# Kernel optimization log

Hardware: AMD Instinct MI355X
Metric: run time of the kernel (lower is better)

## Reference

```python
import jax, jax.numpy as jnp
import numpy as np

B, D, N, L, H, T = 256, 768, 256, 2, 8, 20
HD = D // H

def _ln(x, g, b):
    m = x.mean(-1, keepdims=True)
    v = ((x - m) ** 2).mean(-1, keepdims=True)
    return (x - m) / jnp.sqrt(v + 1e-5) * g + b

def setup_inputs() -> dict:
    key = jax.random.key(0)
    ks = jax.random.split(key, 8)
    kk = jax.random.split(ks[7], 10)
    def w(k, shape):
        return jax.random.normal(k, shape, jnp.float32) * 0.02
    return {
        'feats': jax.random.normal(ks[0], (B, D, N), jnp.float32),
        'past': jax.random.normal(ks[1], (B, 16, 6), jnp.float32),
        'w_qinit': w(ks[2], (121, D)), 'b_qinit': jnp.zeros((D,), jnp.float32),
        'pos_enc': w(ks[3], (1, N, D)),
        'w_pp': w(ks[4], (2, D)), 'b_pp': jnp.zeros((D,), jnp.float32),
        'g_pp': jnp.ones((D,), jnp.float32), 'be_pp': jnp.zeros((D,), jnp.float32),
        'time_emb': w(ks[5], (T, D)),
        'Wq': w(kk[0], (L, D, D)), 'bq': jnp.zeros((L, D), jnp.float32),
        'Wk': w(kk[1], (L, D, D)), 'bk': jnp.zeros((L, D), jnp.float32),
        'Wv': w(kk[2], (L, D, D)), 'bv': jnp.zeros((L, D), jnp.float32),
        'Wo': w(kk[3], (L, D, D)), 'bo': jnp.zeros((L, D), jnp.float32),
        'ln1_g': jnp.ones((L, D), jnp.float32), 'ln1_b': jnp.zeros((L, D), jnp.float32),
        'W1': w(kk[4], (L, D, 4 * D)), 'b1': jnp.zeros((L, 4 * D), jnp.float32),
        'W2': w(kk[5], (L, 4 * D, D)), 'b2': jnp.zeros((L, D), jnp.float32),
        'ln2_g': jnp.ones((L, D), jnp.float32), 'ln2_b': jnp.zeros((L, D), jnp.float32),
        'w_dec1': w(kk[6], (D, D)), 'b_dec1': jnp.zeros((D,), jnp.float32),
        'w_dec2': w(kk[7], (D, 2)), 'b_dec2': jnp.zeros((2,), jnp.float32),
        'intent': jax.random.randint(ks[6], (B,), 0, 3),
    }

def reference(feats, past, w_qinit, b_qinit, pos_enc, w_pp, b_pp, g_pp, be_pp,
              time_emb, Wq, bq, Wk, bk, Wv, bv, Wo, bo, ln1_g, ln1_b,
              W1, b1, W2, b2, ln2_g, ln2_b, w_dec1, b_dec1, w_dec2, b_dec2, intent):
    # tokens: [B, N, D]
    tokens = jnp.transpose(feats, (0, 2, 1)) + pos_enc
    onehot = jax.nn.one_hot(jnp.clip(intent - 1, 0, 2), 3, dtype=tokens.dtype)
    past_flat = past.reshape(B, -1)
    pad = jnp.zeros((B, 22), tokens.dtype)
    context = jnp.concatenate([onehot, past_flat, pad], axis=1) @ w_qinit + b_qinit  # [B, D]
    # precompute cross-attention K/V once per layer (tokens are constant across steps)
    Kh = (jnp.einsum('bnd,lde->lbne', tokens, Wk) + bk[:, None, None, :]).reshape(L, B, N, H, HD)
    Vh = (jnp.einsum('bnd,lde->lbne', tokens, Wv) + bv[:, None, None, :]).reshape(L, B, N, H, HD)
    scale = 1.0 / np.sqrt(HD)

    def step(carry, te):
        ctx, cp = carry
        pq = jax.nn.relu(_ln(cp @ w_pp + b_pp, g_pp, be_pp))
        x = (ctx + pq + te)[:, None, :]  # [B, 1, D]
        for l in range(L):
            q = (_ln(x, ln1_g[l], ln1_b[l]) @ Wq[l] + bq[l]).reshape(B, 1, H, HD)
            s = jnp.einsum('bqhd,bnhd->bhqn', q, Kh[l]) * scale
            a = jax.nn.softmax(s, axis=-1)
            o = jnp.einsum('bhqn,bnhd->bqhd', a, Vh[l]).reshape(B, 1, D) @ Wo[l] + bo[l]
            x = x + o
            h = jax.nn.gelu(_ln(x, ln2_g[l], ln2_b[l]) @ W1[l] + b1[l], approximate=False) @ W2[l] + b2[l]
            x = x + h
        ctx = x[:, 0]
        delta = jax.nn.gelu(ctx @ w_dec1 + b_dec1, approximate=False) @ w_dec2 + b_dec2
        cp = cp + delta
        return (ctx, cp), cp

    init = (context, past[:, -1, 0:2])
    _, ys = jax.lax.scan(step, init, time_emb)  # ys: [T, B, 2]
    return jnp.transpose(ys, (1, 0, 2))
```

## Files before the change

kernel.cpp:

```cpp
#include <hip/hip_runtime.h>
#include <hip/hip_bf16.h>
#include <math.h>

#define B_ 256
#define D_ 768
#define N_ 256
#define L_ 2
#define H_ 8
#define T_ 20
#define HD_ 96
#define D4_ 3072

typedef float f32x4v __attribute__((ext_vector_type(4)));
typedef __bf16 bf16x8v __attribute__((ext_vector_type(8)));

union V16 { uint4 u; bf16x8v v; };

__device__ __forceinline__ ushort f2b(float f) {
    union { float f; unsigned u; } x{f};
    unsigned r = x.u + 0x7fffu + ((x.u >> 16) & 1u);
    return (ushort)(r >> 16);
}
__device__ __forceinline__ float b2f(ushort s) {
    union { unsigned u; float f; } x{(unsigned)s << 16};
    return x.f;
}
__device__ __forceinline__ float gelu_f(float v) {
    return 0.5f * v * (1.0f + erff(v * 0.7071067811865476f));
}
__device__ __forceinline__ float dot8(const float* __restrict__ xp, uint4 u) {
    return xp[0] * b2f((ushort)(u.x & 0xffffu)) + xp[1] * b2f((ushort)(u.x >> 16))
         + xp[2] * b2f((ushort)(u.y & 0xffffu)) + xp[3] * b2f((ushort)(u.y >> 16))
         + xp[4] * b2f((ushort)(u.z & 0xffffu)) + xp[5] * b2f((ushort)(u.z >> 16))
         + xp[6] * b2f((ushort)(u.w & 0xffffu)) + xp[7] * b2f((ushort)(u.w >> 16));
}
__device__ __forceinline__ float blockSum(float v, float* red, int tid) {
    for (int off = 32; off; off >>= 1) v += __shfl_down(v, off, 64);
    int w = tid >> 6, lane = tid & 63;
    if (lane == 0) red[w] = v;
    __syncthreads();
    float r = red[0] + red[1] + red[2] + red[3];
    __syncthreads();
    return r;
}
__device__ __forceinline__ void gl_lds16(const ushort* g, ushort* l) {
    __builtin_amdgcn_global_load_lds((const __attribute__((address_space(1))) unsigned int*)g,
                                     (__attribute__((address_space(3))) unsigned int*)l,
                                     16, 0, 0);
}

__global__ __launch_bounds__(256) void context_kernel(const float* __restrict__ past,
                                                      const float* __restrict__ w_qinit,
                                                      const float* __restrict__ b_qinit,
                                                      const int* __restrict__ intent,
                                                      const float* __restrict__ w_pp,
                                                      const float* __restrict__ b_pp,
                                                      const float* __restrict__ g_pp,
                                                      const float* __restrict__ be_pp,
                                                      const float* __restrict__ te0,
                                                      float* __restrict__ x,
                                                      float* __restrict__ cp) {
    int b = blockIdx.x, tid = threadIdx.x;
    __shared__ float ps[96];
    __shared__ int oidx;
    __shared__ float red[4];
    if (tid < 96) ps[tid] = past[b * 96 + tid];
    if (tid == 0) {
        int iv = intent[b] - 1;
        oidx = iv < 0 ? 0 : (iv > 2 ? 2 : iv);
    }
    __syncthreads();
    float ctx[3];
    #pragma unroll
    for (int r = 0; r < 3; ++r) {
        int d = tid + r * 256;
        float acc = w_qinit[oidx * D_ + d] + b_qinit[d];
        #pragma unroll 8
        for (int p = 0; p < 96; ++p) acc += ps[p] * w_qinit[(3 + p) * D_ + d];
        ctx[r] = acc;
    }
    float c0 = ps[90], c1 = ps[91];
    if (tid == 0) { cp[b * 2] = c0; cp[b * 2 + 1] = c1; }
    float t[3];
    float s = 0, ss = 0;
    #pragma unroll
    for (int r = 0; r < 3; ++r) {
        int d = tid + r * 256;
        t[r] = c0 * w_pp[d] + c1 * w_pp[D_ + d] + b_pp[d];
        s += t[r]; ss += t[r] * t[r];
    }
    s = blockSum(s, red, tid);
    ss = blockSum(ss, red, tid);
    float mean = s * (1.0f / D_);
    float var = ss * (1.0f / D_) - mean * mean;
    float rinv = rsqrtf(var + 1e-5f);
    #pragma unroll
    for (int r = 0; r < 3; ++r) {
        int d = tid + r * 256;
        float pq = fmaxf((t[r] - mean) * rinv * g_pp[d] + be_pp[d], 0.0f);
        x[b * D_ + d] = ctx[r] + pq + te0[d];
    }
}

__global__ __launch_bounds__(256) void token_prep(const float* __restrict__ feats,
                                                  const float* __restrict__ pos_enc,
                                                  ushort* __restrict__ tokens) {
    int b = blockIdx.z;
    int d0 = blockIdx.x * 64, n0 = blockIdx.y * 64;
    __shared__ float tile[64][65];
    int tid = threadIdx.x;
    int nl = tid & 63, dl0 = tid >> 6;
    const float* fb = feats + ((size_t)b * D_ + d0) * N_ + n0;
    #pragma unroll
    for (int i = 0; i < 16; ++i) {
        int dl = dl0 + i * 4;
        tile[dl][nl] = fb[(size_t)dl * N_ + nl];
    }
    __syncthreads();
    int dq = (tid & 15) * 4;
    int ng = tid >> 4;
    #pragma unroll
    for (int i = 0; i < 4; ++i) {
        int nl2 = ng + i * 16;
        int n = n0 + nl2;
        float4 p = *(const float4*)(pos_enc + (size_t)n * D_ + d0 + dq);
        ushort4 o;
        o.x = f2b(tile[dq + 0][nl2] + p.x);
        o.y = f2b(tile[dq + 1][nl2] + p.y);
        o.z = f2b(tile[dq + 2][nl2] + p.z);
        o.w = f2b(tile[dq + 3][nl2] + p.w);
        *(ushort4*)&tokens[((size_t)b * N_ + n) * D_ + d0 + dq] = o;
    }
}

__global__ __launch_bounds__(256) void transpose_w(const float* __restrict__ W,
                                                   ushort* __restrict__ out,
                                                   const float* __restrict__ scale,
                                                   int K, int N) {
    __shared__ float t[32][33];
    int k0 = blockIdx.y * 32, n0 = blockIdx.x * 32;
    int tx = threadIdx.x & 31, ty = threadIdx.x >> 5;
    #pragma unroll
    for (int i = 0; i < 4; ++i)
        t[ty + i * 8][tx] = W[(size_t)(k0 + ty + i * 8) * N + n0 + tx];
    __syncthreads();
    #pragma unroll
    for (int i = 0; i < 4; ++i) {
        int n = n0 + ty + i * 8, k = k0 + tx;
        float v = t[tx][ty + i * 8];
        if (scale) v *= scale[k];
        out[(size_t)n * K + k] = f2b(v);
    }
}

__global__ __launch_bounds__(256) void bias_eff_kernel(const float* __restrict__ W,
                                                       const float* __restrict__ bias,
                                                       const float* __restrict__ lb,
                                                       float* __restrict__ be, int Nc) {
    __shared__ float lbs[768];
    __shared__ float part[4][64];
    int tid = threadIdx.x;
    for (int i = tid; i < 768; i += 256) lbs[i] = lb[i];
    __syncthreads();
    int n0 = blockIdx.x * 64;
    int nl = tid & 63, kp = tid >> 6;
    int n = n0 + nl;
    float a = 0.0f;
    #pragma unroll 4
    for (int k = kp * 192; k < kp * 192 + 192; ++k)
        a += lbs[k] * W[(size_t)k * Nc + n];
    part[kp][nl] = a;
    __syncthreads();
    if (tid < 64)
        be[n0 + tid] = bias[n0 + tid] + part[0][tid] + part[1][tid] + part[2][tid] + part[3][tid];
}

__global__ void kvbias_prep(const float* __restrict__ bk, const float* __restrict__ bv,
                            float* __restrict__ bc) {
    int i = blockIdx.x * 256 + threadIdx.x;
    int mi = i / D_, c = i % D_;
    int l = mi >> 1;
    bc[i] = (mi & 1 ? bv : bk)[l * D_ + c];
}

__global__ __launch_bounds__(256) void kv_gemm_mfma(const ushort* __restrict__ tokens,
                                                    const ushort* __restrict__ Wkvt,
                                                    const float* __restrict__ bias_kv,
                                                    ushort* __restrict__ Kt,
                                                    ushort* __restrict__ Vt) {
    int e0 = blockIdx.x * 128;
    int mi = e0 / D_;
    int ein = e0 % D_;
    int l = mi >> 1, isV = mi & 1;
    int m0 = blockIdx.y * 128;
    int b = m0 >> 8, ntok0 = m0 & 255;
    __shared__ __align__(16) ushort smem[17408];
    int tid = threadIdx.x;
    int w = tid >> 6, lane = tid & 63, quad = lane >> 4, l16 = lane & 15;
    int wr = w >> 1, wc = w & 1;
    int swz = (l16 >> 1) & 3;
    int rchunk = ((quad ^ swz) & 3) * 8;
    f32x4v acc[4][4];
    #pragma unroll
    for (int i = 0; i < 4; ++i)
        #pragma unroll
        for (int j = 0; j < 4; ++j) acc[i][j] = (f32x4v)(0.0f);

    auto stage = [&](int buf, int k0) {
        ushort* Ab = smem + buf * 8192;
        ushort* Bb = Ab + 4096;
        #pragma unroll
        for (int vv = 0; vv < 2; ++vv) {
            int v = tid + vv * 256;
            int row = v >> 2;
            int kq = (v & 3) ^ ((row >> 1) & 3);
            gl_lds16(&tokens[(size_t)(m0 + row) * D_ + k0 + kq * 8], Ab + w * 512 + vv * 2048);
            gl_lds16(&Wkvt[(size_t)(e0 + row) * D_ + k0 + kq * 8],   Bb + w * 512 + vv * 2048);
        }
    };

    stage(0, 0);
    asm volatile("s_waitcnt vmcnt(0)" ::: "memory");
    __syncthreads();
    int cur = 0;
    for (int k0 = 0; k0 < D_; k0 += 32) {
        if (k0 + 32 < D_) stage(cur ^ 1, k0 + 32);
        const ushort* Ab = smem + cur * 8192;
        const ushort* Bb = Ab + 4096;
        V16 a[4], bb[4];
        #pragma unroll
        for (int i = 0; i < 4; ++i)
            a[i].u = *(const uint4*)&Ab[(wr * 64 + i * 16 + l16) * 32 + rchunk];
        #pragma unroll
        for (int j = 0; j < 4; ++j)
            bb[j].u = *(const uint4*)&Bb[(wc * 64 + j * 16 + l16) * 32 + rchunk];
        #pragma unroll
        for (int i = 0; i < 4; ++i)
            #pragma unroll
            for (int j = 0; j < 4; ++j)
                acc[i][j] = __builtin_amdgcn_mfma_f32_16x16x32_bf16(a[i].v, bb[j].v, acc[i][j], 0, 0, 0);
        asm volatile("s_waitcnt vmcnt(0)" ::: "memory");
        __syncthreads();
        cur ^= 1;
    }

    float bcol[4];
    #pragma unroll
    for (int j = 0; j < 4; ++j)
        bcol[j] = bias_kv[e0 + wc * 64 + j * 16 + l16];

    ushort* Ct = smem;
    ushort* outbuf = isV ? Vt : Kt;
    #pragma unroll
    for (int i = 0; i < 4; ++i)
        #pragma unroll
        for (int j = 0; j < 4; ++j) {
            int e_l = wc * 64 + j * 16 + l16;
            int m_b = wr * 64 + i * 16 + quad * 4;
            ushort4 p;
            p.x = f2b(acc[i][j][0] + bcol[j]);
            p.y = f2b(acc[i][j][1] + bcol[j]);
            p.z = f2b(acc[i][j][2] + bcol[j]);
            p.w = f2b(acc[i][j][3] + bcol[j]);
            *(ushort4*)&Ct[e_l * 136 + m_b] = p;
        }
    __syncthreads();
    int e_l = tid >> 1, half = tid & 1;
    int c = ein + e_l;
    int h = c / HD_, hd = c % HD_;
    size_t dst = ((((size_t)l * B_ + b) * H_ + h) * HD_ + hd) * N_ + ntok0 + half * 64;
    #pragma unroll
    for (int p8 = 0; p8 < 8; ++p8)
        *(uint4*)&outbuf[dst + p8 * 8] = *(const uint4*)&Ct[e_l * 136 + half * 64 + p8 * 8];
}

template<int AVAR, int OMODE, int STATS, int KSPLIT>
__global__ __launch_bounds__(256) void gemm_s(const void* __restrict__ Av,
                                              const ushort* __restrict__ Bt,
                                              const float* __restrict__ bias,
                                              void* __restrict__ Cv,
                                              int K, int Nc) {
    __shared__ __align__(16) ushort As[2][2048];
    __shared__ __align__(16) ushort Bs[2][2048];
    __shared__ float smst[64][2];
    int tid = threadIdx.x;
    int m0 = blockIdx.y * 64, e0 = blockIdx.x * 64;
    int kslice = K / KSPLIT;
    int kbeg = blockIdx.z * kslice, kend = kbeg + kslice;
    int w = tid >> 6, lane = tid & 63, quad = lane >> 4, l16 = lane & 15;
    int swz = (l16 >> 1) & 3;
    int rchunk = ((quad ^ swz) & 3) * 8;

    if (STATS) {
        int row = tid >> 2, part = tid & 3;
        const float* xr = (const float*)Av + (size_t)(m0 + row) * K + part * 192;
        float s = 0, ss = 0;
        #pragma unroll 4
        for (int i = 0; i < 192; i += 4) {
            float4 f = *(const float4*)(xr + i);
            s += f.x + f.y + f.z + f.w;
            ss += f.x * f.x + f.y * f.y + f.z * f.z + f.w * f.w;
        }
        s += __shfl_xor(s, 1, 64);  s += __shfl_xor(s, 2, 64);
        ss += __shfl_xor(ss, 1, 64); ss += __shfl_xor(ss, 2, 64);
        if (part == 0) {
            float mean = s * (1.0f / 768.0f);
            float var = ss * (1.0f / 768.0f) - mean * mean;
            smst[row][0] = mean;
            smst[row][1] = rsqrtf(var + 1e-5f);
        }
        __syncthreads();
    }

    bool doA = w < 2;
    int t2 = tid & 127;
    f32x4v acc[4];
    #pragma unroll
    for (int i = 0; i < 4; ++i) acc[i] = (f32x4v)(0.0f);

    auto fetchA1 = [&](int kk, int vv) -> uint4 {
        int v = t2 + vv * 128;
        int row = v >> 2, kq = v & 3;
        const float* Af = (const float*)Av + (size_t)(m0 + row) * K + kk + kq * 8;
        float4 f0 = *(const float4*)Af;
        float4 f1 = *(const float4*)(Af + 4);
        float mn = smst[row][0], rs = smst[row][1];
        f0.x = (f0.x - mn) * rs; f0.y = (f0.y - mn) * rs;
        f0.z = (f0.z - mn) * rs; f0.w = (f0.w - mn) * rs;
        f1.x = (f1.x - mn) * rs; f1.y = (f1.y - mn) * rs;
        f1.z = (f1.z - mn) * rs; f1.w = (f1.w - mn) * rs;
        uint4 u;
        u.x = (unsigned)f2b(f0.x) | ((unsigned)f2b(f0.y) << 16);
        u.y = (unsigned)f2b(f0.z) | ((unsigned)f2b(f0.w) << 16);
        u.z = (unsigned)f2b(f1.x) | ((unsigned)f2b(f1.y) << 16);
        u.w = (unsigned)f2b(f1.z) | ((unsigned)f2b(f1.w) << 16);
        return u;
    };
    auto stashA = [&](int buf, int vv, uint4 u) {
        int v = t2 + vv * 128;
        int row = v >> 2, kq = v & 3;
        *(uint4*)&As[buf][row * 32 + ((kq ^ ((row >> 1) & 3)) & 3) * 8] = u;
    };
    auto stageA0 = [&](int buf, int kk) {
        #pragma unroll
        for (int vv = 0; vv < 2; ++vv) {
            int v = t2 + vv * 128;
            int row = v >> 2;
            int kq = (v & 3) ^ ((row >> 1) & 3);
            gl_lds16((const ushort*)Av + (size_t)(m0 + row) * K + kk + kq * 8,
                     &As[buf][w * 512 + vv * 1024]);
        }
    };
    auto stageB = [&](int buf, int kk) {
        int wb = w - 2;
        #pragma unroll
        for (int vv = 0; vv < 2; ++vv) {
            int v = t2 + vv * 128;
            int row = v >> 2;
            int kq = (v & 3) ^ ((row >> 1) & 3);
            gl_lds16(&Bt[(size_t)(e0 + row) * K + kk + kq * 8],
                     &Bs[buf][wb * 512 + vv * 1024]);
        }
    };
    auto compute = [&](int buf) {
        V16 bb;
        bb.u = *(const uint4*)&Bs[buf][(w * 16 + l16) * 32 + rchunk];
        #pragma unroll
        for (int i = 0; i < 4; ++i) {
            V16 a;
            a.u = *(const uint4*)&As[buf][(i * 16 + l16) * 32 + rchunk];
            acc[i] = __builtin_amdgcn_mfma_f32_16x16x32_bf16(a.v, bb.v, acc[i], 0, 0, 0);
        }
    };

    if (doA) {
        if (AVAR == 0) {
            stageA0(0, kbeg);
        } else {
            uint4 p0 = fetchA1(kbeg, 0), p1 = fetchA1(kbeg, 1);
            stashA(0, 0, p0); stashA(0, 1, p1);
        }
    } else {
        stageB(0, kbeg);
    }
    asm volatile("s_waitcnt vmcnt(0)" ::: "memory");
    __syncthreads();
    int cur = 0;
    for (int kk = kbeg + 32; kk < kend; kk += 32) {
        uint4 p0, p1;
        if (doA) {
            if (AVAR == 0) stageA0(cur ^ 1, kk);
            else { p0 = fetchA1(kk, 0); p1 = fetchA1(kk, 1); }
        } else {
            stageB(cur ^ 1, kk);
        }
        compute(cur);
        if (AVAR == 1 && doA) { stashA(cur ^ 1, 0, p0); stashA(cur ^ 1, 1, p1); }
        asm volatile("s_waitcnt vmcnt(0)" ::: "memory");
        __syncthreads();
        cur ^= 1;
    }
    compute(cur);

    int n = e0 + w * 16 + l16;
    float bn = 0.0f;
    if (OMODE != 2 || blockIdx.z == 0) bn = bias[n];
    #pragma unroll
    for (int i = 0; i < 4; ++i) {
        #pragma unroll
        for (int r = 0; r < 4; ++r) {
            int m = m0 + i * 16 + quad * 4 + r;
            float v = acc[i][r] + bn;
            if (OMODE == 1) v = gelu_f(v);
            if (OMODE == 2) atomicAdd((float*)Cv + (size_t)m * Nc + n, v);
            else            ((ushort*)Cv)[(size_t)m * Nc + n] = f2b(v);
        }
    }
}

__global__ __launch_bounds__(256) void attn_fused(const float* __restrict__ x,
                                                  const ushort* __restrict__ Wqt,
                                                  const float* __restrict__ bqe,
                                                  const ushort* __restrict__ Kt,
                                                  const ushort* __restrict__ Vt,
                                                  ushort* __restrict__ att) {
    int b = blockIdx.y, h = blockIdx.x, tid = threadIdx.x;
    int w = tid >> 6, lane = tid & 63;
    __shared__ float xs[768];
    __shared__ float red[4];
    __shared__ float qs[96];
    __shared__ float spart[4][256];
    __shared__ float sc[256];
    __shared__ float opo[96];

    if (tid < 192) *(float4*)&xs[tid * 4] = *(const float4*)&x[(size_t)b * D_ + tid * 4];
    __syncthreads();

    float s = 0, ss = 0;
    #pragma unroll
    for (int r = 0; r < 3; ++r) { float v = xs[tid + r * 256]; s += v; ss += v * v; }
    s = blockSum(s, red, tid);
    ss = blockSum(ss, red, tid);
    float mean = s * (1.0f / D_);
    float var = ss * (1.0f / D_) - mean * mean;
    float rinv = rsqrtf(var + 1e-5f);
    #pragma unroll
    for (int r = 0; r < 3; ++r) { int d = tid + r * 256; xs[d] = (xs[d] - mean) * rinv; }
    __syncthreads();

    if (tid < 192) {
        int j = tid >> 1, kh = tid & 1;
        const ushort* wr = Wqt + (size_t)(h * HD_ + j) * D_ + kh * 384;
        const float* xp = xs + kh * 384;
        float acc = 0.0f;
        #pragma unroll 4
        for (int k = 0; k < 384; k += 8)
            acc += dot8(xp + k, *(const uint4*)&wr[k]);
        acc += __shfl_xor(acc, 1, 64);
        if (kh == 0) qs[j] = (acc + bqe[h * HD_ + j]) * 0.10206207261596575f;
    }
    __syncthreads();

    {
        int r2 = lane >> 5, tg = lane & 31;
        const ushort* Kp = Kt + (size_t)(b * H_ + h) * HD_ * N_;
        float s8[8];
        #pragma unroll
        for (int j = 0; j < 8; ++j) s8[j] = 0.0f;
        #pragma unroll 4
        for (int i = 0; i < 12; ++i) {
            int hd = w * 24 + i * 2 + r2;
            uint4 kk = *(const uint4*)&Kp[hd * N_ + tg * 8];
            float qv = qs[hd];
            s8[0] += qv * b2f((ushort)(kk.x & 0xffffu));
            s8[1] += qv * b2f((ushort)(kk.x >> 16));
            s8[2] += qv * b2f((ushort)(kk.y & 0xffffu));
            s8[3] += qv * b2f((ushort)(kk.y >> 16));
            s8[4] += qv * b2f((ushort)(kk.z & 0xffffu));
            s8[5] += qv * b2f((ushort)(kk.z >> 16));
            s8[6] += qv * b2f((ushort)(kk.w & 0xffffu));
            s8[7] += qv * b2f((ushort)(kk.w >> 16));
        }
        #pragma unroll
        for (int j = 0; j < 8; ++j) s8[j] += __shfl_xor(s8[j], 32, 64);
        if (r2 == 0) {
            float4 lo, hi;
            lo.x = s8[0]; lo.y = s8[1]; lo.z = s8[2]; lo.w = s8[3];
            hi.x = s8[4]; hi.y = s8[5]; hi.z = s8[6]; hi.w = s8[7];
            *(float4*)&spart[w][tg * 8] = lo;
            *(float4*)&spart[w][tg * 8 + 4] = hi;
        }
    }
    __syncthreads();

    float sv = spart[0][tid] + spart[1][tid] + spart[2][tid] + spart[3][tid];
    float m = sv;
    for (int off = 32; off; off >>= 1) m = fmaxf(m, __shfl_xor(m, off, 64));
    if (lane == 0) red[w] = m;
    __syncthreads();
    m = fmaxf(fmaxf(red[0], red[1]), fmaxf(red[2], red[3]));
    __syncthreads();
    float e = expf(sv - m);
    float tot = blockSum(e, red, tid);
    sc[tid] = e / tot;
    __syncthreads();

    if (tid < 192) {
        int hd = tid >> 1, nh = tid & 1;
        const ushort* Vr = Vt + (size_t)(b * H_ + h) * HD_ * N_ + hd * N_ + nh * 128;
        const float* scp = sc + nh * 128;
        float o = 0.0f;
        #pragma unroll 4
        for (int i = 0; i < 16; ++i)
            o += dot8(scp + i * 8, *(const uint4*)&Vr[i * 8]);
        o += __shfl_xor(o, 1, 64);
        if (nh == 0) opo[hd] = o;
    }
    __syncthreads();
    if (tid < 96) att[(size_t)b * D_ + h * HD_ + tid] = f2b(opo[tid]);
}

__global__ __launch_bounds__(256) void tail_kernel(float* __restrict__ x,
                                                   const ushort* __restrict__ dec1t,
                                                   const float* __restrict__ b_dec1,
                                                   const float* __restrict__ w_dec2,
                                                   const float* __restrict__ b_dec2,
                                                   float* __restrict__ cp,
                                                   float* __restrict__ out,
                                                   const float* __restrict__ time_emb,
                                                   const float* __restrict__ w_pp,
                                                   const float* __restrict__ b_pp,
                                                   const float* __restrict__ g_pp,
                                                   const float* __restrict__ be_pp,
                                                   int t) {
    int b = blockIdx.x, tid = threadIdx.x;
    __shared__ float xs[768];
    __shared__ float red[4];
    #pragma unroll
    for (int r = 0; r < 3; ++r) xs[tid + r * 256] = x[b * D_ + tid + r * 256];
    __syncthreads();
    float d0 = 0, d1 = 0, d2 = 0;
    const ushort* w0 = dec1t + (size_t)tid * D_;
    const ushort* w1 = w0 + (size_t)256 * D_;
    const ushort* w2 = w0 + (size_t)512 * D_;
    #pragma unroll 2
    for (int k = 0; k < 768; k += 8) {
        d0 += dot8(xs + k, *(const uint4*)&w0[k]);
        d1 += dot8(xs + k, *(const uint4*)&w1[k]);
        d2 += dot8(xs + k, *(const uint4*)&w2[k]);
    }
    float v0 = gelu_f(d0 + b_dec1[tid]);
    float v1 = gelu_f(d1 + b_dec1[tid + 256]);
    float v2 = gelu_f(d2 + b_dec1[tid + 512]);
    float p0 = v0 * w_dec2[tid * 2]     + v1 * w_dec2[(tid + 256) * 2]     + v2 * w_dec2[(tid + 512) * 2];
    float p1 = v0 * w_dec2[tid * 2 + 1] + v1 * w_dec2[(tid + 256) * 2 + 1] + v2 * w_dec2[(tid + 512) * 2 + 1];
    p0 = blockSum(p0, red, tid);
    p1 = blockSum(p1, red, tid);
    float c0 = cp[b * 2] + p0 + b_dec2[0];
    float c1 = cp[b * 2 + 1] + p1 + b_dec2[1];
    if (tid == 0) {
        cp[b * 2] = c0;
        cp[b * 2 + 1] = c1;
        out[(b * T_ + t) * 2] = c0;
        out[(b * T_ + t) * 2 + 1] = c1;
    }
    if (t < T_ - 1) {
        const float* te = time_emb + (size_t)(t + 1) * D_;
        float tv[3];
        float s = 0, ss = 0;
        #pragma unroll
        for (int r = 0; r < 3; ++r) {
            int d = tid + r * 256;
            tv[r] = c0 * w_pp[d] + c1 * w_pp[D_ + d] + b_pp[d];
            s += tv[r]; ss += tv[r] * tv[r];
        }
        s = blockSum(s, red, tid);
        ss = blockSum(ss, red, tid);
        float mean = s * (1.0f / D_);
        float var = ss * (1.0f / D_) - mean * mean;
        float rinv = rsqrtf(var + 1e-5f);
        #pragma unroll
        for (int r = 0; r < 3; ++r) {
            int d = tid + r * 256;
            float pq = fmaxf((tv[r] - mean) * rinv * g_pp[d] + be_pp[d], 0.0f);
            x[b * D_ + d] += pq + te[d];
        }
    }
}

extern "C" void kernel_launch(void* const* d_in, const int* in_sizes, int n_in,
                              void* d_out, int out_size, void* d_ws, size_t ws_size,
                              hipStream_t stream) {
    const float* feats   = (const float*)d_in[0];
    const float* past    = (const float*)d_in[1];
    const float* w_qinit = (const float*)d_in[2];
    const float* b_qinit = (const float*)d_in[3];
    const float* pos_enc = (const float*)d_in[4];
    const float* w_pp    = (const float*)d_in[5];
    const float* b_pp    = (const float*)d_in[6];
    const float* g_pp    = (const float*)d_in[7];
    const float* be_pp   = (const float*)d_in[8];
    const float* time_emb= (const float*)d_in[9];
    const float* Wq      = (const float*)d_in[10];
    const float* bq      = (const float*)d_in[11];
    const float* Wk      = (const float*)d_in[12];
    const float* bk      = (const float*)d_in[13];
    const float* Wv      = (const float*)d_in[14];
    const float* bv      = (const float*)d_in[15];
    const float* Wo      = (const float*)d_in[16];
    const float* bo      = (const float*)d_in[17];
    const float* ln1_g   = (const float*)d_in[18];
    const float* ln1_b   = (const float*)d_in[19];
    const float* W1      = (const float*)d_in[20];
    const float* b1      = (const float*)d_in[21];
    const float* W2      = (const float*)d_in[22];
    const float* b2      = (const float*)d_in[23];
    const float* ln2_g   = (const float*)d_in[24];
    const float* ln2_b   = (const float*)d_in[25];
    const float* w_dec1  = (const float*)d_in[26];
    const float* b_dec1  = (const float*)d_in[27];
    const float* w_dec2  = (const float*)d_in[28];
    const float* b_dec2  = (const float*)d_in[29];
    const int*   intent  = (const int*)d_in[30];
    float* out = (float*)d_out;

    const size_t WD = (size_t)D_ * D_;
    const size_t WD4 = (size_t)D_ * D4_;
    const size_t kv_elems = (size_t)L_ * B_ * H_ * HD_ * N_;
    const size_t kv_l = (size_t)B_ * H_ * HD_ * N_;

    char* wp = (char*)d_ws;
    ushort* Kt     = (ushort*)wp; wp += kv_elems * 2;
    ushort* Vt     = (ushort*)wp; wp += kv_elems * 2;
    ushort* tokens = (ushort*)wp; wp += (size_t)B_ * N_ * D_ * 2;
    ushort* Wkvt   = (ushort*)wp; wp += 4 * WD * 2;
    ushort* Wqt    = (ushort*)wp; wp += 2 * WD * 2;
    ushort* Wot    = (ushort*)wp; wp += 2 * WD * 2;
    ushort* W1t    = (ushort*)wp; wp += 2 * WD4 * 2;
    ushort* W2t    = (ushort*)wp; wp += 2 * WD4 * 2;
    ushort* dec1t  = (ushort*)wp; wp += WD * 2;
    float* bias_kv = (float*)wp;  wp += 4 * D_ * 4;
    float* bqe     = (float*)wp;  wp += 2 * D_ * 4;
    float* b1e     = (float*)wp;  wp += 2 * D4_ * 4;
    float* x       = (float*)wp;  wp += (size_t)B_ * D_ * 4;
    ushort* attbuf = (ushort*)wp; wp += (size_t)B_ * D_ * 2;
    ushort* h1     = (ushort*)wp; wp += (size_t)B_ * D4_ * 2;
    float* cp      = (float*)wp;  wp += (size_t)B_ * 2 * 4;

    context_kernel<<<B_, 256, 0, stream>>>(past, w_qinit, b_qinit, intent,
                                           w_pp, b_pp, g_pp, be_pp, time_emb, x, cp);
    token_prep<<<dim3(12, 4, 256), 256, 0, stream>>>(feats, pos_enc, tokens);
    kvbias_prep<<<12, 256, 0, stream>>>(bk, bv, bias_kv);
    for (int l = 0; l < L_; ++l) {
        transpose_w<<<dim3(24, 24), 256, 0, stream>>>(Wk + l * WD, Wkvt + (2 * l + 0) * WD, nullptr, D_, D_);
        transpose_w<<<dim3(24, 24), 256, 0, stream>>>(Wv + l * WD, Wkvt + (2 * l + 1) * WD, nullptr, D_, D_);
        transpose_w<<<dim3(24, 24), 256, 0, stream>>>(Wq + l * WD, Wqt + l * WD, ln1_g + l * D_, D_, D_);
        transpose_w<<<dim3(24, 24), 256, 0, stream>>>(Wo + l * WD, Wot + l * WD, nullptr, D_, D_);
        transpose_w<<<dim3(96, 24), 256, 0, stream>>>(W1 + l * WD4, W1t + l * WD4, ln2_g + l * D_, D_, D4_);
        transpose_w<<<dim3(24, 96), 256, 0, stream>>>(W2 + l * WD4, W2t + l * WD4, nullptr, D4_, D_);
        bias_eff_kernel<<<12, 256, 0, stream>>>(Wq + l * WD, bq + l * D_, ln1_b + l * D_, bqe + l * D_, D_);
        bias_eff_kernel<<<48, 256, 0, stream>>>(W1 + l * WD4, b1 + l * D4_, ln2_b + l * D_, b1e + l * D4_, D4_);
    }
    transpose_w<<<dim3(24, 24), 256, 0, stream>>>(w_dec1, dec1t, nullptr, D_, D_);

    kv_gemm_mfma<<<dim3(24, 512), 256, 0, stream>>>(tokens, Wkvt, bias_kv, Kt, Vt);

    for (int t = 0; t < T_; ++t) {
        for (int l = 0; l < L_; ++l) {
            attn_fused<<<dim3(H_, B_), 256, 0, stream>>>(x, Wqt + l * WD, bqe + l * D_,
                                                         Kt + l * kv_l, Vt + l * kv_l, attbuf);
            gemm_s<0, 2, 0, 4><<<dim3(12, 4, 4), 256, 0, stream>>>(attbuf, Wot + l * WD,
                                                                   bo + l * D_, x, D_, D_);
            gemm_s<1, 1, 1, 1><<<dim3(48, 4), 256, 0, stream>>>(x, W1t + l * WD4,
                                                                b1e + l * D4_, h1, D_, D4_);
            gemm_s<0, 2, 0, 4><<<dim3(12, 4, 4), 256, 0, stream>>>(h1, W2t + l * WD4,
                                                                   b2 + l * D_, x, D4_, D_);
        }
        tail_kernel<<<B_, 256, 0, stream>>>(x, dec1t, b_dec1, w_dec2, b_dec2, cp, out,
                                            time_emb, w_pp, b_pp, g_pp, be_pp, t);
    }
}
```

Measured before the change: 6.794 ms.

## Fuse attention output projection into attention kernel using double-buffered residual

Moves the Wo projection into attn_fused: each head block multiplies its 96-dim output by its slice of Wo and atomically adds the result into a second residual buffer. This removes one GEMM launch per layer and the bf16 attention buffer. Keeping two residual copies (xA/xB) consistent takes extra writes in context, tail, the W1 stats pass and a dual atomic in the W2 epilogue. The kv_gemm LDS swizzle is also removed, which may bring back bank conflicts. Each attention block now reads Wo with many scalar-heavy dot products and issues three fp32 atomics per thread.

```diff
diff --git a/kernel.cpp b/kernel.cpp
--- a/kernel.cpp
+++ b/kernel.cpp
@@ -58,7 +58,8 @@
                                                       const float* __restrict__ g_pp,
                                                       const float* __restrict__ be_pp,
                                                       const float* __restrict__ te0,
-                                                      float* __restrict__ x,
+                                                      float* __restrict__ xA,
+                                                      float* __restrict__ xB,
                                                       float* __restrict__ cp) {
     int b = blockIdx.x, tid = threadIdx.x;
     __shared__ float ps[96];
@@ -98,7 +99,9 @@
     for (int r = 0; r < 3; ++r) {
         int d = tid + r * 256;
         float pq = fmaxf((t[r] - mean) * rinv * g_pp[d] + be_pp[d], 0.0f);
-        x[b * D_ + d] = ctx[r] + pq + te0[d];
+        float nv = ctx[r] + pq + te0[d];
+        xA[b * D_ + d] = nv;
+        xB[b * D_ + d] = nv;
     }
 }
 
@@ -198,8 +201,6 @@
     int tid = threadIdx.x;
     int w = tid >> 6, lane = tid & 63, quad = lane >> 4, l16 = lane & 15;
     int wr = w >> 1, wc = w & 1;
-    int swz = (l16 >> 1) & 3;
-    int rchunk = ((quad ^ swz) & 3) * 8;
     f32x4v acc[4][4];
     #pragma unroll
     for (int i = 0; i < 4; ++i)
@@ -212,10 +213,9 @@
         #pragma unroll
         for (int vv = 0; vv < 2; ++vv) {
             int v = tid + vv * 256;
-            int row = v >> 2;
-            int kq = (v & 3) ^ ((row >> 1) & 3);
-            gl_lds16(&tokens[(size_t)(m0 + row) * D_ + k0 + kq * 8], Ab + w * 512 + vv * 2048);
-            gl_lds16(&Wkvt[(size_t)(e0 + row) * D_ + k0 + kq * 8],   Bb + w * 512 + vv * 2048);
+            int row = v >> 2, kv = v & 3;
+            gl_lds16(&tokens[(size_t)(m0 + row) * D_ + k0 + kv * 8], Ab + w * 512 + vv * 2048);
+            gl_lds16(&Wkvt[(size_t)(e0 + row) * D_ + k0 + kv * 8],   Bb + w * 512 + vv * 2048);
         }
     };
 
@@ -230,10 +230,10 @@
         V16 a[4], bb[4];
         #pragma unroll
         for (int i = 0; i < 4; ++i)
-            a[i].u = *(const uint4*)&Ab[(wr * 64 + i * 16 + l16) * 32 + rchunk];
+            a[i].u = *(const uint4*)&Ab[(wr * 64 + i * 16 + l16) * 32 + quad * 8];
         #pragma unroll
         for (int j = 0; j < 4; ++j)
-            bb[j].u = *(const uint4*)&Bb[(wc * 64 + j * 16 + l16) * 32 + rchunk];
+            bb[j].u = *(const uint4*)&Bb[(wc * 64 + j * 16 + l16) * 32 + quad * 8];
         #pragma unroll
         for (int i = 0; i < 4; ++i)
             #pragma unroll
@@ -279,6 +279,8 @@
                                               const ushort* __restrict__ Bt,
                                               const float* __restrict__ bias,
                                               void* __restrict__ Cv,
+                                              float* __restrict__ Cv2,
+                                              float* __restrict__ xcopy,
                                               int K, int Nc) {
     __shared__ __align__(16) ushort As[2][2048];
     __shared__ __align__(16) ushort Bs[2][2048];
@@ -294,10 +296,13 @@
     if (STATS) {
         int row = tid >> 2, part = tid & 3;
         const float* xr = (const float*)Av + (size_t)(m0 + row) * K + part * 192;
+        float* xc = xcopy ? xcopy + (size_t)(m0 + row) * K + part * 192 : nullptr;
+        bool doCopy = xcopy && blockIdx.x == 0;
         float s = 0, ss = 0;
         #pragma unroll 4
         for (int i = 0; i < 192; i += 4) {
             float4 f = *(const float4*)(xr + i);
+            if (doCopy) *(float4*)(xc + i) = f;
             s += f.x + f.y + f.z + f.w;
             ss += f.x * f.x + f.y * f.y + f.z * f.z + f.w * f.w;
         }
@@ -412,18 +417,24 @@
             int m = m0 + i * 16 + quad * 4 + r;
             float v = acc[i][r] + bn;
             if (OMODE == 1) v = gelu_f(v);
-            if (OMODE == 2) atomicAdd((float*)Cv + (size_t)m * Nc + n, v);
-            else            ((ushort*)Cv)[(size_t)m * Nc + n] = f2b(v);
-        }
-    }
-}
-
-__global__ __launch_bounds__(256) void attn_fused(const float* __restrict__ x,
+            if (OMODE == 2) {
+                atomicAdd((float*)Cv + (size_t)m * Nc + n, v);
+                if (Cv2) atomicAdd(Cv2 + (size_t)m * Nc + n, v);
+            } else {
+                ((ushort*)Cv)[(size_t)m * Nc + n] = f2b(v);
+            }
+        }
+    }
+}
+
+__global__ __launch_bounds__(256) void attn_fused(const float* __restrict__ xin,
                                                   const ushort* __restrict__ Wqt,
                                                   const float* __restrict__ bqe,
                                                   const ushort* __restrict__ Kt,
                                                   const ushort* __restrict__ Vt,
-                                                  ushort* __restrict__ att) {
+                                                  const ushort* __restrict__ Wot,
+                                                  const float* __restrict__ bo,
+                                                  float* __restrict__ xout) {
     int b = blockIdx.y, h = blockIdx.x, tid = threadIdx.x;
     int w = tid >> 6, lane = tid & 63;
     __shared__ float xs[768];
@@ -433,7 +444,7 @@
     __shared__ float sc[256];
     __shared__ float opo[96];
 
-    if (tid < 192) *(float4*)&xs[tid * 4] = *(const float4*)&x[(size_t)b * D_ + tid * 4];
+    if (tid < 192) *(float4*)&xs[tid * 4] = *(const float4*)&xin[(size_t)b * D_ + tid * 4];
     __syncthreads();
 
     float s = 0, ss = 0;
@@ -517,10 +528,23 @@
         if (nh == 0) opo[hd] = o;
     }
     __syncthreads();
-    if (tid < 96) att[(size_t)b * D_ + h * HD_ + tid] = f2b(opo[tid]);
-}
-
-__global__ __launch_bounds__(256) void tail_kernel(float* __restrict__ x,
+
+    #pragma unroll
+    for (int r = 0; r < 3; ++r) {
+        int n = tid + r * 256;
+        const ushort* wr = Wot + (size_t)n * D_ + h * HD_;
+        float a = 0.0f;
+        #pragma unroll
+        for (int j8 = 0; j8 < 12; ++j8)
+            a += dot8(opo + j8 * 8, *(const uint4*)&wr[j8 * 8]);
+        if (h == 0) a += bo[n];
+        atomicAdd(&xout[(size_t)b * D_ + n], a);
+    }
+}
+
+__global__ __launch_bounds__(256) void tail_kernel(const float* __restrict__ xB,
+                                                   float* __restrict__ xA,
+                                                   float* __restrict__ xB2,
                                                    const ushort* __restrict__ dec1t,
                                                    const float* __restrict__ b_dec1,
                                                    const float* __restrict__ w_dec2,
@@ -537,7 +561,7 @@
     __shared__ float xs[768];
     __shared__ float red[4];
     #pragma unroll
-    for (int r = 0; r < 3; ++r) xs[tid + r * 256] = x[b * D_ + tid + r * 256];
+    for (int r = 0; r < 3; ++r) xs[tid + r * 256] = xB[b * D_ + tid + r * 256];
     __syncthreads();
     float d0 = 0, d1 = 0, d2 = 0;
     const ushort* w0 = dec1t + (size_t)tid * D_;
@@ -583,7 +607,9 @@
         for (int r = 0; r < 3; ++r) {
             int d = tid + r * 256;
             float pq = fmaxf((tv[r] - mean) * rinv * g_pp[d] + be_pp[d], 0.0f);
-            x[b * D_ + d] += pq + te[d];
+            float nv = xs[tid + r * 256] + pq + te[d];
+            xA[b * D_ + d] = nv;
+            xB2[b * D_ + d] = nv;
         }
     }
 }
@@ -642,13 +668,13 @@
     float* bias_kv = (float*)wp;  wp += 4 * D_ * 4;
     float* bqe     = (float*)wp;  wp += 2 * D_ * 4;
     float* b1e     = (float*)wp;  wp += 2 * D4_ * 4;
-    float* x       = (float*)wp;  wp += (size_t)B_ * D_ * 4;
-    ushort* attbuf = (ushort*)wp; wp += (size_t)B_ * D_ * 2;
+    float* xA      = (float*)wp;  wp += (size_t)B_ * D_ * 4;
+    float* xB      = (float*)wp;  wp += (size_t)B_ * D_ * 4;
     ushort* h1     = (ushort*)wp; wp += (size_t)B_ * D4_ * 2;
     float* cp      = (float*)wp;  wp += (size_t)B_ * 2 * 4;
 
     context_kernel<<<B_, 256, 0, stream>>>(past, w_qinit, b_qinit, intent,
-                                           w_pp, b_pp, g_pp, be_pp, time_emb, x, cp);
+                                           w_pp, b_pp, g_pp, be_pp, time_emb, xA, xB, cp);
     token_prep<<<dim3(12, 4, 256), 256, 0, stream>>>(feats, pos_enc, tokens);
     kvbias_prep<<<12, 256, 0, stream>>>(bk, bv, bias_kv);
     for (int l = 0; l < L_; ++l) {
@@ -667,16 +693,15 @@
 
     for (int t = 0; t < T_; ++t) {
         for (int l = 0; l < L_; ++l) {
-            attn_fused<<<dim3(H_, B_), 256, 0, stream>>>(x, Wqt + l * WD, bqe + l * D_,
-                                                         Kt + l * kv_l, Vt + l * kv_l, attbuf);
-            gemm_s<0, 2, 0, 4><<<dim3(12, 4, 4), 256, 0, stream>>>(attbuf, Wot + l * WD,
-                                                                   bo + l * D_, x, D_, D_);
-            gemm_s<1, 1, 1, 1><<<dim3(48, 4), 256, 0, stream>>>(x, W1t + l * WD4,
-                                                                b1e + l * D4_, h1, D_, D4_);
+            attn_fused<<<dim3(H_, B_), 256, 0, stream>>>(xA, Wqt + l * WD, bqe + l * D_,
+                                                         Kt + l * kv_l, Vt + l * kv_l,
+                                                         Wot + l * WD, bo + l * D_, xB);
+            gemm_s<1, 1, 1, 1><<<dim3(48, 4), 256, 0, stream>>>(xB, W1t + l * WD4,
+                                                                b1e + l * D4_, h1, nullptr, xA, D_, D4_);
             gemm_s<0, 2, 0, 4><<<dim3(12, 4, 4), 256, 0, stream>>>(h1, W2t + l * WD4,
-                                                                   b2 + l * D_, x, D4_, D_);
-        }
-        tail_kernel<<<B_, 256, 0, stream>>>(x, dec1t, b_dec1, w_dec2, b_dec2, cp, out,
+                                                                   b2 + l * D_, xB, xA, nullptr, D4_, D_);
+        }
+        tail_kernel<<<B_, 256, 0, stream>>>(xB, xA, xB, dec1t, b_dec1, w_dec2, b_dec2, cp, out,
                                             time_emb, w_pp, b_pp, g_pp, be_pp, t);
     }
 }
```

New measurement: 8.379 ms. 23.3% more time.

## Triple-buffer KV GEMM LDS staging and drop XOR swizzle

Applied to the files above, without the earlier changes.

Switches the K/V projection GEMM from double-buffered to triple-buffered LDS staging, prefetching two K-tiles ahead and waiting with a partial vmcnt so global loads overlap more compute. It also removes the XOR swizzle on the LDS layout and reads fragments at plain quad offsets. This raises shared memory per block, which may lower occupancy, and the unswizzled layout may reintroduce LDS bank conflicts.

```diff
diff --git a/kernel.cpp b/kernel.cpp
--- a/kernel.cpp
+++ b/kernel.cpp
@@ -194,12 +194,10 @@
     int l = mi >> 1, isV = mi & 1;
     int m0 = blockIdx.y * 128;
     int b = m0 >> 8, ntok0 = m0 & 255;
-    __shared__ __align__(16) ushort smem[17408];
+    __shared__ __align__(16) ushort smem[24576];
     int tid = threadIdx.x;
     int w = tid >> 6, lane = tid & 63, quad = lane >> 4, l16 = lane & 15;
     int wr = w >> 1, wc = w & 1;
-    int swz = (l16 >> 1) & 3;
-    int rchunk = ((quad ^ swz) & 3) * 8;
     f32x4v acc[4][4];
     #pragma unroll
     for (int i = 0; i < 4; ++i)
@@ -212,37 +210,46 @@
         #pragma unroll
         for (int vv = 0; vv < 2; ++vv) {
             int v = tid + vv * 256;
-            int row = v >> 2;
-            int kq = (v & 3) ^ ((row >> 1) & 3);
-            gl_lds16(&tokens[(size_t)(m0 + row) * D_ + k0 + kq * 8], Ab + w * 512 + vv * 2048);
-            gl_lds16(&Wkvt[(size_t)(e0 + row) * D_ + k0 + kq * 8],   Bb + w * 512 + vv * 2048);
+            int row = v >> 2, kv = v & 3;
+            gl_lds16(&tokens[(size_t)(m0 + row) * D_ + k0 + kv * 8], Ab + w * 512 + vv * 2048);
+            gl_lds16(&Wkvt[(size_t)(e0 + row) * D_ + k0 + kv * 8],   Bb + w * 512 + vv * 2048);
         }
     };
-
-    stage(0, 0);
-    asm volatile("s_waitcnt vmcnt(0)" ::: "memory");
-    __syncthreads();
-    int cur = 0;
-    for (int k0 = 0; k0 < D_; k0 += 32) {
-        if (k0 + 32 < D_) stage(cur ^ 1, k0 + 32);
-        const ushort* Ab = smem + cur * 8192;
+    auto compute = [&](int buf) {
+        const ushort* Ab = smem + buf * 8192;
         const ushort* Bb = Ab + 4096;
         V16 a[4], bb[4];
         #pragma unroll
         for (int i = 0; i < 4; ++i)
-            a[i].u = *(const uint4*)&Ab[(wr * 64 + i * 16 + l16) * 32 + rchunk];
+            a[i].u = *(const uint4*)&Ab[(wr * 64 + i * 16 + l16) * 32 + quad * 8];
         #pragma unroll
         for (int j = 0; j < 4; ++j)
-            bb[j].u = *(const uint4*)&Bb[(wc * 64 + j * 16 + l16) * 32 + rchunk];
+            bb[j].u = *(const uint4*)&Bb[(wc * 64 + j * 16 + l16) * 32 + quad * 8];
         #pragma unroll
         for (int i = 0; i < 4; ++i)
             #pragma unroll
             for (int j = 0; j < 4; ++j)
                 acc[i][j] = __builtin_amdgcn_mfma_f32_16x16x32_bf16(a[i].v, bb[j].v, acc[i][j], 0, 0, 0);
-        asm volatile("s_waitcnt vmcnt(0)" ::: "memory");
-        __syncthreads();
-        cur ^= 1;
-    }
+    };
+
+    stage(0, 0);
+    stage(1, 32);
+    asm volatile("s_waitcnt vmcnt(4)" ::: "memory");
+    __syncthreads();
+    #define NT_ (D_ / 32)
+    for (int t = 0; t < NT_; ++t) {
+        if (t + 2 < NT_) stage((t + 2) % 3, (t + 2) * 32);
+        compute(t % 3);
+        if (t + 2 < NT_) {
+            asm volatile("s_waitcnt vmcnt(4)" ::: "memory");
+            __syncthreads();
+        } else if (t + 1 < NT_) {
+            asm volatile("s_waitcnt vmcnt(0)" ::: "memory");
+            __syncthreads();
+        }
+    }
+    #undef NT_
+    __syncthreads();
 
     float bcol[4];
     #pragma unroll
```

Result: no change. 6.697 ms (-1.4%).
